# Performance work log

Hardware: AMD Instinct MI355X
Metric: run time of the kernel (lower is better)

## Reference

```python
import jax, jax.numpy as jnp
import numpy as np

R = 3                 # search_radius
S2 = (2 * R + 1) ** 2  # 49 correlation channels
VIS_PIXEL_SCALE = 0.1  # arcsec / pixel


def _interp_tokens(tokens, sh, sw, dh, dw):
    # tokens [B, N, D] on (sh, sw) grid -> (dh, dw) grid
    B, N, D = tokens.shape
    x = jnp.transpose(tokens, (0, 2, 1)).reshape(B, D, sh, sw)
    if (sh, sw) != (dh, dw):
        # torch F.interpolate bilinear align_corners=False == jax half-pixel bilinear
        x = jax.image.resize(x, (B, D, dh, dw), method='bilinear')
    return x  # [B, D, dh, dw]


def _l2norm(x, eps=1e-12):
    n = jnp.sqrt(jnp.sum(x * x, axis=1, keepdims=True))
    return x / jnp.maximum(n, eps)


def _corr_volume(q, ref):
    # q, ref: [B, D, H, W]; local cosine-similarity volume [B, S2, H, W]
    q = _l2norm(q)
    ref = _l2norm(ref)
    B, D, H, W = q.shape
    refp = jnp.pad(ref, ((0, 0), (0, 0), (R, R), (R, R)), mode='edge')  # replicate pad
    slices = [
        jnp.sum(q * jax.lax.dynamic_slice(refp, (0, 0, R + dy, R + dx), (B, D, H, W)), axis=1)
        for dy in range(-R, R + 1) for dx in range(-R, R + 1)
    ]
    return jnp.stack(slices, axis=1)


def _conv5(x, w, b):
    y = jax.lax.conv_general_dilated(x, w, (1, 1), 'SAME',
                                     dimension_numbers=('NCHW', 'OIHW', 'NCHW'))
    return y + b[None, :, None, None]


def _refine_net(x, w0, b0, w1, b1, w2, b2):
    h = jax.nn.gelu(_conv5(x, w0, b0), approximate=False)
    h = jax.nn.gelu(_conv5(h, w1, b1), approximate=False)
    return _conv5(h, w2, b2)


def setup_inputs() -> dict:
    key = jax.random.key(0)
    ks = jax.random.split(key, 8)
    B, D = 4, 256
    rubin_tokens = jax.random.normal(ks[0], (B, 64 * 64, D), dtype=jnp.float32)
    vis_tokens = jax.random.normal(ks[1], (B, 128 * 128, D), dtype=jnp.float32)
    in_ch = 2 + S2 + 1  # 52
    hid = 32
    def kaiming(k, shape):
        fan_in = shape[1] * shape[2] * shape[3]
        return jax.random.normal(k, shape, dtype=jnp.float32) / np.sqrt(fan_in)
    w0 = kaiming(ks[2], (hid, in_ch, 5, 5)); b0 = jnp.zeros((hid,), jnp.float32)
    w1 = kaiming(ks[3], (hid, hid, 5, 5));   b1 = jnp.zeros((hid,), jnp.float32)
    w2 = kaiming(ks[4], (2, hid, 5, 5));     b2 = jnp.zeros((2,), jnp.float32)
    log_temp = jnp.asarray(np.log(0.1), dtype=jnp.float32)
    return {
        'rubin_tokens': rubin_tokens, 'vis_tokens': vis_tokens,
        'w0': w0, 'b0': b0, 'w1': w1, 'b1': b1, 'w2': w2, 'b2': b2,
        'log_temp': log_temp,
        'rubin_h': 64, 'rubin_w': 64, 'vis_h': 128, 'vis_w': 128,
        'img_h': 2048, 'img_w': 2048,
    }


def reference(rubin_tokens, vis_tokens, w0, b0, w1, b1, w2, b2, log_temp,
              rubin_h, rubin_w, vis_h, vis_w, img_h, img_w):
    Hc, Wc = max(rubin_h, vis_h), max(rubin_w, vis_w)
    q = _interp_tokens(rubin_tokens, rubin_h, rubin_w, Hc, Wc)  # [B,D,Hc,Wc]
    k = _interp_tokens(vis_tokens, vis_h, vis_w, Hc, Wc)
    corr = _corr_volume(q, k)  # [B,S2,Hc,Wc]

    # soft-argmax over the (2R+1)^2 neighborhood
    coords = jnp.arange(-R, R + 1, dtype=corr.dtype)
    cy, cx = jnp.meshgrid(coords, coords, indexing='ij')
    cy = cy.reshape(1, S2, 1, 1)
    cx = cx.reshape(1, S2, 1, 1)
    temp = jnp.exp(log_temp)
    weights = jax.nn.softmax(corr / temp, axis=1)
    dy = jnp.sum(weights * cy, axis=1, keepdims=True)
    dx = jnp.sum(weights * cx, axis=1, keepdims=True)
    confidence = jnp.max(weights, axis=1, keepdims=True)
    raw_offsets = jnp.concatenate([dy, dx], axis=1)  # [B,2,Hc,Wc]

    x = jnp.concatenate([raw_offsets, corr, confidence], axis=1)  # [B,52,Hc,Wc]
    residual = _refine_net(x, w0, b0, w1, b1, w2, b2)
    refined = raw_offsets + residual

    sky_per_token_y = img_h * VIS_PIXEL_SCALE / Hc
    sky_per_token_x = img_w * VIS_PIXEL_SCALE / Wc
    dra = refined[:, 1:2] * sky_per_token_x
    ddec = refined[:, 0:1] * sky_per_token_y
    # [B,5,Hc,Wc]: dra, ddec, raw_dy, raw_dx, confidence
    return jnp.concatenate([dra, ddec, dy, dx, confidence], axis=1)
```

## Files before the change

kernel.cpp:

```cpp
#include <hip/hip_runtime.h>
#include <math.h>

#define Hh 128
#define Ww 128
#define Dd 256
#define Bb 4
#define HW (Hh*Ww)
#define NPIX (Bb*HW)
#define WP 132

typedef __attribute__((ext_vector_type(8))) short s16x8;
typedef __attribute__((ext_vector_type(4))) float f32x4;

__device__ __forceinline__ unsigned short f2bf(float f) {
    unsigned u = __float_as_uint(f);
    u += 0x7FFF + ((u >> 16) & 1);
    return (unsigned short)(u >> 16);
}

__device__ __forceinline__ float gelu_exact(float v) {
    return 0.5f * v * (1.0f + erff(v * 0.70710678118654752f));
}

__device__ __forceinline__ void ring_yx(int i, int& y, int& x) {
    if (i < 264) { y = i / 132; x = i - y * 132; }
    else if (i < 528) { int j = i - 264; int r = j / 132; y = 130 + r; x = j - r * 132; }
    else { int j = i - 528; y = 2 + (j >> 2); int m = j & 3; x = (m < 2) ? m : 128 + m; }
}

__global__ __launch_bounds__(256) void setup_norm(const float* __restrict__ w0,
                                                  const float* __restrict__ w1,
                                                  const float* __restrict__ w2,
                                                  unsigned short* __restrict__ wb0,
                                                  unsigned short* __restrict__ wb1,
                                                  unsigned short* __restrict__ wb2,
                                                  unsigned short* __restrict__ xbp,
                                                  unsigned short* __restrict__ h1p,
                                                  unsigned short* __restrict__ h2p,
                                                  const float* __restrict__ vis,
                                                  const float* __restrict__ rub,
                                                  unsigned short* __restrict__ kn,
                                                  unsigned short* __restrict__ qn) {
    __shared__ float stok[36 * 260];
    int tid = threadIdx.x;
    int blk = blockIdx.x;
    if (blk < 610) {
        int t = blk * 256 + tid;
        if (t < 66560) {
            uint4 z = (uint4){0, 0, 0, 0};
            if (t < 33280) {
                int img = t / 8320; int r = t - img * 8320; int px = r >> 3, g = r & 7;
                int y, x; ring_yx(px, y, x);
                *(uint4*)(xbp + ((size_t)(img * WP + y) * WP + x) * 64 + g * 8) = z;
            } else {
                int u = t - 33280;
                unsigned short* base = (u < 16640) ? h1p : h2p;
                int v = (u < 16640) ? u : u - 16640;
                int img = v / 4160; int r = v - img * 4160; int px = r >> 2, g = r & 3;
                int y, x; ring_yx(px, y, x);
                *(uint4*)(base + ((size_t)(img * WP + y) * WP + x) * 32 + g * 8) = z;
            }
            return;
        }
        int u = t - 66560;
        if (u < 51200) {
            int tap = u >> 11; int r = u & 2047; int n = r >> 6; int k = r & 63;
            wb0[u] = (k < 52) ? f2bf(w0[n * 1300 + k * 25 + tap]) : (unsigned short)0;
        } else if (u < 76800) {
            int v = u - 51200; int tap = v >> 10; int r = v & 1023; int n = r >> 5; int k = r & 31;
            wb1[v] = f2bf(w1[n * 800 + k * 25 + tap]);
        } else if (u < 89600) {
            int v = u - 76800; int tap = v >> 9; int r = v & 511; int n = r >> 5; int k = r & 31;
            wb2[v] = (n < 2) ? f2bf(w2[n * 800 + k * 25 + tap]) : (unsigned short)0;
        }
        return;
    }
    int nb = blk - 610;
    int g16 = tid >> 4, l = tid & 15;
    if (nb < 4096) {
        int pix = nb * 16 + g16;
        const float* base = vis + (size_t)pix * Dd + l * 4;
        float4 v[4];
#pragma unroll
        for (int i = 0; i < 4; i++) v[i] = *(const float4*)(base + i * 64);
        float ss = 0.f;
#pragma unroll
        for (int i = 0; i < 4; i++)
            ss += v[i].x * v[i].x + v[i].y * v[i].y + v[i].z * v[i].z + v[i].w * v[i].w;
#pragma unroll
        for (int o = 1; o <= 8; o <<= 1) ss += __shfl_xor(ss, o, 64);
        float inv = __builtin_amdgcn_rsqf(fmaxf(ss, 1e-24f));
        unsigned short* op = kn + (size_t)pix * Dd + l * 4;
#pragma unroll
        for (int i = 0; i < 4; i++) {
            ushort4 o4;
            o4.x = f2bf(v[i].x * inv); o4.y = f2bf(v[i].y * inv);
            o4.z = f2bf(v[i].z * inv); o4.w = f2bf(v[i].w * inv);
            *(ushort4*)(op + i * 64) = o4;
        }
    } else {
        int blk2 = nb - 4096;
        int b = blk2 >> 8;
        int rem = blk2 & 255;
        int ty = rem >> 4, tx = rem & 15;
        int oy0 = ty * 8, ox0 = tx * 8;
        int rb = ty * 4 - 1, cb = tx * 4 - 1;
#pragma unroll
        for (int i = 0; i < 9; i++) {
            int g = i * 256 + tid;
            int t = g >> 6, c = g & 63;
            int jy = t / 6, jx = t - jy * 6;
            int gy = min(max(rb + jy, 0), 63);
            int gx = min(max(cb + jx, 0), 63);
            *(float4*)&stok[t * 260 + c * 4] =
                *(const float4*)(rub + ((size_t)(b * 4096 + gy * 64 + gx)) * 256 + c * 4);
        }
        __syncthreads();
        for (int k = 0; k < 4; k++) {
            int pp = g16 * 4 + k;
            int r = pp >> 3, c2 = pp & 7;
            int yo = oy0 + r, xo = ox0 + c2;
            float sy = 0.5f * yo - 0.25f, sx = 0.5f * xo - 0.25f;
            float fyf = floorf(sy), fxf = floorf(sx);
            float fy = sy - fyf, fx = sx - fxf;
            int jy0 = (int)fyf - rb, jx0 = (int)fxf - cb;
            const float* t00 = &stok[(jy0 * 6 + jx0) * 260 + l * 4];
            const float* t01 = t00 + 260;
            const float* t10 = t00 + 6 * 260;
            const float* t11 = t10 + 260;
            float w00 = (1.f - fy) * (1.f - fx), w01 = (1.f - fy) * fx;
            float w10 = fy * (1.f - fx), w11 = fy * fx;
            float4 bv[4];
            float ss = 0.f;
#pragma unroll
            for (int i = 0; i < 4; i++) {
                float4 a = *(const float4*)(t00 + i * 64);
                float4 b1 = *(const float4*)(t01 + i * 64);
                float4 c = *(const float4*)(t10 + i * 64);
                float4 d = *(const float4*)(t11 + i * 64);
                float4 v;
                v.x = w00 * a.x + w01 * b1.x + w10 * c.x + w11 * d.x;
                v.y = w00 * a.y + w01 * b1.y + w10 * c.y + w11 * d.y;
                v.z = w00 * a.z + w01 * b1.z + w10 * c.z + w11 * d.z;
                v.w = w00 * a.w + w01 * b1.w + w10 * c.w + w11 * d.w;
                bv[i] = v;
                ss += v.x * v.x + v.y * v.y + v.z * v.z + v.w * v.w;
            }
#pragma unroll
            for (int o = 1; o <= 8; o <<= 1) ss += __shfl_xor(ss, o, 64);
            float inv = __builtin_amdgcn_rsqf(fmaxf(ss, 1e-24f));
            size_t pix = (size_t)(b << 14) + yo * 128 + xo;
            unsigned short* op = qn + pix * Dd + l * 4;
#pragma unroll
            for (int i = 0; i < 4; i++) {
                ushort4 o4;
                o4.x = f2bf(bv[i].x * inv); o4.y = f2bf(bv[i].y * inv);
                o4.z = f2bf(bv[i].z * inv); o4.w = f2bf(bv[i].w * inv);
                *(ushort4*)(op + i * 64) = o4;
            }
        }
    }
}

__global__ __launch_bounds__(512, 4) void corr_block(const unsigned short* __restrict__ qn,
                                                     const unsigned short* __restrict__ kn,
                                                     const float* __restrict__ log_temp,
                                                     unsigned short* __restrict__ xb,
                                                     float* __restrict__ out) {
    constexpr int ASMEM = 308 * 5 * 16;
    __shared__ char smem[ASMEM + 128 * 65 * 4];
    unsigned* sC = (unsigned*)(smem + ASMEM);
    int tid = threadIdx.x;
    int wid = tid >> 6, lane = tid & 63, l15 = lane & 15, quad = lane >> 4;
    int blk = blockIdx.x;
    int b = blk >> 7, rem = blk & 127;
    int y0 = (rem >> 3) << 3, x0 = (rem & 7) << 4;
    int y = y0 + wid;

#pragma unroll
    for (int i = 0; i < 3; i++) {
        int g = i * 512 + tid;
        int px = g / 12, ch = 52 + g - (g / 12) * 12;
        sC[px * 65 + ch] = 0u;
    }

    const unsigned short* src0; int dst0;
    const unsigned short* src1; int dst1;
    const unsigned short* src2; int dst2; bool hav2;
    {
        int g = tid;
        int px = g >> 2, sub = g & 3;
        int ry = px / 22, rx = px - ry * 22;
        int yy = min(max(y0 - 3 + ry, 0), 127);
        int xx = min(max(x0 - 3 + rx, 0), 127);
        src0 = kn + ((size_t)(b << 14) + yy * 128 + xx) * 256 + sub * 8;
        dst0 = (px * 5 + sub) * 16;
        g = 512 + tid;
        px = g >> 2; sub = g & 3;
        ry = px / 22; rx = px - ry * 22;
        yy = min(max(y0 - 3 + ry, 0), 127);
        xx = min(max(x0 - 3 + rx, 0), 127);
        src1 = kn + ((size_t)(b << 14) + yy * 128 + xx) * 256 + sub * 8;
        dst1 = (px * 5 + sub) * 16;
        g = 1024 + tid;
        hav2 = (g < 1232);
        int gc = hav2 ? g : 1231;
        px = gc >> 2; sub = gc & 3;
        ry = px / 22; rx = px - ry * 22;
        yy = min(max(y0 - 3 + ry, 0), 127);
        xx = min(max(x0 - 3 + rx, 0), 127);
        src2 = kn + ((size_t)(b << 14) + yy * 128 + xx) * 256 + sub * 8;
        dst2 = (px * 5 + sub) * 16;
    }
    int lpixoff[10];
#pragma unroll
    for (int f = 0; f < 10; f++) {
        int p = min(f * 16 + l15, 153);
        int pr = p / 22, pc = p - pr * 22;
        lpixoff[f] = (((wid + pr) * 22 + pc) * 5 + quad) * 16;
    }
    const unsigned short* aptr = qn + ((size_t)(b << 14) + y * 128 + x0 + l15) * 256 + quad * 8;

    f32x4 acc[10];
#pragma unroll
    for (int f = 0; f < 10; f++) acc[f] = (f32x4){0.f, 0.f, 0.f, 0.f};

    uint4 v0 = *(const uint4*)src0;
    uint4 v1 = *(const uint4*)src1;
    uint4 v2 = *(const uint4*)src2;
    s16x8 an = *(const s16x8*)aptr;
    for (int c = 0; c < 8; c++) {
        uint4 w0v = v0, w1v = v1, w2v = v2;
        s16x8 a = an;
        if (c < 7) {
            v0 = *(const uint4*)(src0 + (c + 1) * 32);
            v1 = *(const uint4*)(src1 + (c + 1) * 32);
            v2 = *(const uint4*)(src2 + (c + 1) * 32);
            an = *(const s16x8*)(aptr + (c + 1) * 32);
        }
        __syncthreads();
        *(uint4*)(smem + dst0) = w0v;
        *(uint4*)(smem + dst1) = w1v;
        if (hav2) *(uint4*)(smem + dst2) = w2v;
        __syncthreads();
#pragma unroll
        for (int f = 0; f < 10; f++) {
            s16x8 bf = *(const s16x8*)(smem + lpixoff[f]);
            acc[f] = __builtin_amdgcn_mfma_f32_16x16x32_bf16(a, bf, acc[f], 0, 0, 0);
        }
    }

    float inv_temp = expf(-log_temp[0]);
    float vmax[4] = {-1e30f, -1e30f, -1e30f, -1e30f};
#pragma unroll
    for (int f = 0; f < 10; f++) {
        int n = f * 16 + l15;
        if (n <= 153) {
            int dy = n / 22 - 3;
            int rx = n - (dy + 3) * 22;
#pragma unroll
            for (int i = 0; i < 4; i++) {
                int m = quad * 4 + i;
                int dx = rx - m - 3;
                if ((unsigned)(dx + 3) <= 6u) vmax[i] = fmaxf(vmax[i], acc[f][i]);
            }
        }
    }
#pragma unroll
    for (int o = 1; o <= 8; o <<= 1) {
#pragma unroll
        for (int i = 0; i < 4; i++) vmax[i] = fmaxf(vmax[i], __shfl_xor(vmax[i], o, 64));
    }
    float se[4] = {0, 0, 0, 0}, sey[4] = {0, 0, 0, 0}, sex[4] = {0, 0, 0, 0}, emax[4] = {0, 0, 0, 0};
#pragma unroll
    for (int f = 0; f < 10; f++) {
        int n = f * 16 + l15;
        if (n <= 153) {
            int dy = n / 22 - 3;
            int rx = n - (dy + 3) * 22;
#pragma unroll
            for (int i = 0; i < 4; i++) {
                int m = quad * 4 + i;
                int dx = rx - m - 3;
                if ((unsigned)(dx + 3) <= 6u) {
                    float v = acc[f][i];
                    float e = expf((v - vmax[i]) * inv_temp);
                    se[i] += e;
                    sey[i] += e * (float)dy;
                    sex[i] += e * (float)dx;
                    emax[i] = fmaxf(emax[i], e);
                    sC[(wid * 16 + m) * 65 + 2 + (dy + 3) * 7 + (dx + 3)] = (unsigned)f2bf(v);
                }
            }
        }
    }
#pragma unroll
    for (int o = 1; o <= 8; o <<= 1) {
#pragma unroll
        for (int i = 0; i < 4; i++) {
            se[i] += __shfl_xor(se[i], o, 64);
            sey[i] += __shfl_xor(sey[i], o, 64);
            sex[i] += __shfl_xor(sex[i], o, 64);
            emax[i] = fmaxf(emax[i], __shfl_xor(emax[i], o, 64));
        }
    }
    if (l15 == 0) {
#pragma unroll
        for (int i = 0; i < 4; i++) {
            int m = quad * 4 + i;
            float inv_se = 1.0f / se[i];
            float dyv = sey[i] * inv_se, dxv = sex[i] * inv_se, conf = emax[i] * inv_se;
            int px = wid * 16 + m;
            sC[px * 65 + 0] = (unsigned)f2bf(dyv);
            sC[px * 65 + 1] = (unsigned)f2bf(dxv);
            sC[px * 65 + 51] = (unsigned)f2bf(conf);
            float* op = out + (size_t)b * 5 * HW + y * 128 + x0 + m;
            op[2 * HW] = dyv; op[3 * HW] = dxv; op[4 * HW] = conf;
        }
    }
    __syncthreads();
#pragma unroll
    for (int i = 0; i < 2; i++) {
        int t2 = i * 512 + tid;
        int px = t2 >> 3, seg = t2 & 7;
        const unsigned* sp = sC + px * 65 + seg * 8;
        uint4 o;
        o.x = sp[0] | (sp[1] << 16);
        o.y = sp[2] | (sp[3] << 16);
        o.z = sp[4] | (sp[5] << 16);
        o.w = sp[6] | (sp[7] << 16);
        unsigned short* dst = xb + ((size_t)(b * WP + y0 + (px >> 4) + 2) * WP + x0 + (px & 15) + 2) * 64 + seg * 8;
        *(uint4*)dst = o;
    }
}

template <int KS, int OC, bool GELU>
__global__ __launch_bounds__(512, 4) void conv_tile(const unsigned short* __restrict__ in,
                                                    const unsigned short* __restrict__ wb,
                                                    const float* __restrict__ bias,
                                                    unsigned short* __restrict__ outp) {
    constexpr int ICP = KS * 32;
    constexpr int NF = OC / 16;
    constexpr int ABYTES = 240 * 64;
    constexpr int WROWS = 25 * OC;
    constexpr int WGRAN = WROWS * 4;
    __shared__ char smem[ABYTES + WROWS * 64];
    int tid = threadIdx.x;
    int wv = tid >> 6, lane = tid & 63, l15 = lane & 15, quad = lane >> 4;
    int blk = blockIdx.x;
    int b = blk >> 7, rem = blk & 127;
    int ty = rem >> 3, tx = rem & 7;
    int y0 = ty * 8, x0 = tx * 16;

    f32x4 acc[NF];
#pragma unroll
    for (int g = 0; g < NF; g++) acc[g] = (f32x4){0.f, 0.f, 0.f, 0.f};

    for (int ks = 0; ks < KS; ks++) {
        __syncthreads();
#pragma unroll
        for (int i = 0; i < 2; i++) {
            int g = i * 512 + tid;
            if (g < 960) {
                int px = g >> 2, sub = g & 3;
                int r = px / 20, c = px - r * 20;
                *(uint4*)(smem + px * 64 + (((sub ^ (px >> 1)) & 3) << 4)) =
                    *(const uint4*)(in + ((size_t)(b * WP + y0 + r) * WP + x0 + c) * ICP + ks * 32 + sub * 8);
            }
        }
#pragma unroll
        for (int i = 0; i < (WGRAN + 511) / 512; i++) {
            int g = i * 512 + tid;
            if (g < WGRAN) {
                int nl = g >> 2, sub = g & 3;
                *(uint4*)(smem + ABYTES + nl * 64 + (((sub ^ (nl >> 1)) & 3) << 4)) =
                    *(const uint4*)(wb + (size_t)nl * ICP + ks * 32 + sub * 8);
            }
        }
        __syncthreads();
#pragma unroll
        for (int ky = 0; ky < 5; ky++) {
#pragma unroll
            for (int kx = 0; kx < 5; kx++) {
                int px = (wv + ky) * 20 + l15 + kx;
                s16x8 a = *(const s16x8*)(smem + px * 64 + (((quad ^ (px >> 1)) & 3) << 4));
#pragma unroll
                for (int g = 0; g < NF; g++) {
                    int row = (ky * 5 + kx) * OC + g * 16 + l15;
                    s16x8 bf = *(const s16x8*)(smem + ABYTES + row * 64 + (((quad ^ (row >> 1)) & 3) << 4));
                    acc[g] = __builtin_amdgcn_mfma_f32_16x16x32_bf16(a, bf, acc[g], 0, 0, 0);
                }
            }
        }
    }
    size_t orow = ((size_t)(b * WP + y0 + wv + 2) * WP + x0 + 2) * OC;
#pragma unroll
    for (int g = 0; g < NF; g++) {
        float bv = bias[g * 16 + l15];
#pragma unroll
        for (int r = 0; r < 4; r++) {
            int m = quad * 4 + r;
            float v = acc[g][r] + bv;
            if (GELU) v = gelu_exact(v);
            outp[orow + (size_t)m * OC + g * 16 + l15] = f2bf(v);
        }
    }
}

__global__ __launch_bounds__(512, 4) void conv_final_tile(const unsigned short* __restrict__ in,
                                                          const unsigned short* __restrict__ wb,
                                                          const float* __restrict__ bias,
                                                          float* __restrict__ out) {
    constexpr int ICP = 32, OC = 16;
    constexpr int ABYTES = 240 * 64;
    constexpr int WROWS = 25 * OC;
    constexpr int WGRAN = WROWS * 4;
    __shared__ char smem[ABYTES + WROWS * 64];
    int tid = threadIdx.x;
    int wv = tid >> 6, lane = tid & 63, l15 = lane & 15, quad = lane >> 4;
    int blk = blockIdx.x;
    int b = blk >> 7, rem = blk & 127;
    int ty = rem >> 3, tx = rem & 7;
    int y0 = ty * 8, x0 = tx * 16;

#pragma unroll
    for (int i = 0; i < 2; i++) {
        int g = i * 512 + tid;
        if (g < 960) {
            int px = g >> 2, sub = g & 3;
            int r = px / 20, c = px - r * 20;
            *(uint4*)(smem + px * 64 + (((sub ^ (px >> 1)) & 3) << 4)) =
                *(const uint4*)(in + ((size_t)(b * WP + y0 + r) * WP + x0 + c) * ICP + sub * 8);
        }
    }
#pragma unroll
    for (int i = 0; i < 4; i++) {
        int g = i * 512 + tid;
        if (g < WGRAN) {
            int nl = g >> 2, sub = g & 3;
            *(uint4*)(smem + ABYTES + nl * 64 + (((sub ^ (nl >> 1)) & 3) << 4)) =
                *(const uint4*)(wb + (size_t)nl * ICP + sub * 8);
        }
    }
    __syncthreads();
    f32x4 acc = (f32x4){0.f, 0.f, 0.f, 0.f};
#pragma unroll
    for (int ky = 0; ky < 5; ky++) {
#pragma unroll
        for (int kx = 0; kx < 5; kx++) {
            int px = (wv + ky) * 20 + l15 + kx;
            s16x8 a = *(const s16x8*)(smem + px * 64 + (((quad ^ (px >> 1)) & 3) << 4));
            int row = (ky * 5 + kx) * OC + l15;
            s16x8 bf = *(const s16x8*)(smem + ABYTES + row * 64 + (((quad ^ (row >> 1)) & 3) << 4));
            acc = __builtin_amdgcn_mfma_f32_16x16x32_bf16(a, bf, acc, 0, 0, 0);
        }
    }
    if (l15 < 2) {
        float bv = bias[l15];
#pragma unroll
        for (int r = 0; r < 4; r++) {
            int m = quad * 4 + r;
            size_t p5 = (size_t)b * 5 * HW + (y0 + wv) * Ww + x0 + m;
            float a = acc[r] + bv;
            if (l15 == 0) {
                float dyv = out[p5 + 2 * HW];
                out[p5 + HW] = (dyv + a) * 1.6f;
            } else {
                float dxv = out[p5 + 3 * HW];
                out[p5] = (dxv + a) * 1.6f;
            }
        }
    }
}

extern "C" void kernel_launch(void* const* d_in, const int* in_sizes, int n_in,
                              void* d_out, int out_size, void* d_ws, size_t ws_size,
                              hipStream_t stream) {
    const float* rub = (const float*)d_in[0];
    const float* vis = (const float*)d_in[1];
    const float* w0 = (const float*)d_in[2];
    const float* b0 = (const float*)d_in[3];
    const float* w1 = (const float*)d_in[4];
    const float* b1 = (const float*)d_in[5];
    const float* w2 = (const float*)d_in[6];
    const float* b2 = (const float*)d_in[7];
    const float* log_temp = (const float*)d_in[8];
    float* out = (float*)d_out;

    char* ws = (char*)d_ws;
    size_t off = 0;
    const size_t PADPIX = (size_t)Bb * WP * WP;
    unsigned short* kn = (unsigned short*)(ws + off); off += (size_t)NPIX * Dd * 2;
    unsigned short* qn = (unsigned short*)(ws + off); off += (size_t)NPIX * Dd * 2;
    unsigned short* xbp = (unsigned short*)(ws + off); off += PADPIX * 64 * 2;
    unsigned short* h1p = (unsigned short*)(ws + off); off += PADPIX * 32 * 2;
    unsigned short* h2p = (unsigned short*)(ws + off); off += PADPIX * 32 * 2;
    unsigned short* wb0 = (unsigned short*)(ws + off); off += 51200 * 2;
    unsigned short* wb1 = (unsigned short*)(ws + off); off += 25600 * 2;
    unsigned short* wb2 = (unsigned short*)(ws + off); off += 12800 * 2;

    setup_norm<<<5730, 256, 0, stream>>>(w0, w1, w2, wb0, wb1, wb2,
                                         xbp, h1p, h2p, vis, rub, kn, qn);
    corr_block<<<512, 512, 0, stream>>>(qn, kn, log_temp, xbp, out);
    conv_tile<2, 32, true><<<512, 512, 0, stream>>>(xbp, wb0, b0, h1p);
    conv_tile<1, 32, true><<<512, 512, 0, stream>>>(h1p, wb1, b1, h2p);
    conv_final_tile<<<512, 512, 0, stream>>>(h2p, wb2, b2, out);
}
```

Baseline: 192.0 us.

## Widen correlation K-chunks to 64 and vectorize bf16 normalization stores

The correlation kernel now stages 64 channels of the reference window per step instead of 32, so it makes 4 trips with barriers instead of 8, and issues two MFMAs per fragment per trip. The shared buffer is reused for the sC scratch after an extra barrier, so LDS use drops. The normalization kernels now give each pixel 32 lanes and write packed 16-byte bf16 stores instead of 8-byte ones. The trade-off is more live prefetch registers in the correlation loop and a larger per-step staging footprint.

```diff
diff --git a/kernel.cpp b/kernel.cpp
--- a/kernel.cpp
+++ b/kernel.cpp
@@ -76,28 +76,36 @@
         return;
     }
     int nb = blk - 610;
-    int g16 = tid >> 4, l = tid & 15;
+    int g32 = tid >> 5, l = tid & 31;
     if (nb < 4096) {
-        int pix = nb * 16 + g16;
-        const float* base = vis + (size_t)pix * Dd + l * 4;
-        float4 v[4];
-#pragma unroll
-        for (int i = 0; i < 4; i++) v[i] = *(const float4*)(base + i * 64);
-        float ss = 0.f;
-#pragma unroll
-        for (int i = 0; i < 4; i++)
-            ss += v[i].x * v[i].x + v[i].y * v[i].y + v[i].z * v[i].z + v[i].w * v[i].w;
-#pragma unroll
-        for (int o = 1; o <= 8; o <<= 1) ss += __shfl_xor(ss, o, 64);
-        float inv = __builtin_amdgcn_rsqf(fmaxf(ss, 1e-24f));
-        unsigned short* op = kn + (size_t)pix * Dd + l * 4;
-#pragma unroll
-        for (int i = 0; i < 4; i++) {
-            ushort4 o4;
-            o4.x = f2bf(v[i].x * inv); o4.y = f2bf(v[i].y * inv);
-            o4.z = f2bf(v[i].z * inv); o4.w = f2bf(v[i].w * inv);
-            *(ushort4*)(op + i * 64) = o4;
-        }
+        int pix0 = nb * 16 + g32 * 2;
+        const float* base0 = vis + (size_t)pix0 * Dd + l * 4;
+        float4 a0 = *(const float4*)(base0);
+        float4 b0 = *(const float4*)(base0 + 128);
+        float4 a1 = *(const float4*)(base0 + 256);
+        float4 b1 = *(const float4*)(base0 + 384);
+        float ss0 = a0.x * a0.x + a0.y * a0.y + a0.z * a0.z + a0.w * a0.w +
+                    b0.x * b0.x + b0.y * b0.y + b0.z * b0.z + b0.w * b0.w;
+        float ss1 = a1.x * a1.x + a1.y * a1.y + a1.z * a1.z + a1.w * a1.w +
+                    b1.x * b1.x + b1.y * b1.y + b1.z * b1.z + b1.w * b1.w;
+#pragma unroll
+        for (int o = 1; o <= 16; o <<= 1) {
+            ss0 += __shfl_xor(ss0, o, 64);
+            ss1 += __shfl_xor(ss1, o, 64);
+        }
+        float inv0 = __builtin_amdgcn_rsqf(fmaxf(ss0, 1e-24f));
+        float inv1 = __builtin_amdgcn_rsqf(fmaxf(ss1, 1e-24f));
+        uint4 o0, o1;
+        o0.x = f2bf(a0.x * inv0) | ((unsigned)f2bf(a0.y * inv0) << 16);
+        o0.y = f2bf(a0.z * inv0) | ((unsigned)f2bf(a0.w * inv0) << 16);
+        o0.z = f2bf(b0.x * inv0) | ((unsigned)f2bf(b0.y * inv0) << 16);
+        o0.w = f2bf(b0.z * inv0) | ((unsigned)f2bf(b0.w * inv0) << 16);
+        o1.x = f2bf(a1.x * inv1) | ((unsigned)f2bf(a1.y * inv1) << 16);
+        o1.y = f2bf(a1.z * inv1) | ((unsigned)f2bf(a1.w * inv1) << 16);
+        o1.z = f2bf(b1.x * inv1) | ((unsigned)f2bf(b1.y * inv1) << 16);
+        o1.w = f2bf(b1.z * inv1) | ((unsigned)f2bf(b1.w * inv1) << 16);
+        *(uint4*)(kn + (size_t)pix0 * Dd + l * 8) = o0;
+        *(uint4*)(kn + (size_t)(pix0 + 1) * Dd + l * 8) = o1;
     } else {
         int blk2 = nb - 4096;
         int b = blk2 >> 8;
@@ -116,48 +124,51 @@
                 *(const float4*)(rub + ((size_t)(b * 4096 + gy * 64 + gx)) * 256 + c * 4);
         }
         __syncthreads();
-        for (int k = 0; k < 4; k++) {
-            int pp = g16 * 4 + k;
+        for (int k = 0; k < 8; k++) {
+            int pp = g32 * 8 + k;
             int r = pp >> 3, c2 = pp & 7;
             int yo = oy0 + r, xo = ox0 + c2;
             float sy = 0.5f * yo - 0.25f, sx = 0.5f * xo - 0.25f;
             float fyf = floorf(sy), fxf = floorf(sx);
             float fy = sy - fyf, fx = sx - fxf;
             int jy0 = (int)fyf - rb, jx0 = (int)fxf - cb;
-            const float* t00 = &stok[(jy0 * 6 + jx0) * 260 + l * 4];
+            const float* t00 = &stok[(jy0 * 6 + jx0) * 260];
             const float* t01 = t00 + 260;
             const float* t10 = t00 + 6 * 260;
             const float* t11 = t10 + 260;
             float w00 = (1.f - fy) * (1.f - fx), w01 = (1.f - fy) * fx;
             float w10 = fy * (1.f - fx), w11 = fy * fx;
-            float4 bv[4];
-            float ss = 0.f;
-#pragma unroll
-            for (int i = 0; i < 4; i++) {
-                float4 a = *(const float4*)(t00 + i * 64);
-                float4 b1 = *(const float4*)(t01 + i * 64);
-                float4 c = *(const float4*)(t10 + i * 64);
-                float4 d = *(const float4*)(t11 + i * 64);
-                float4 v;
-                v.x = w00 * a.x + w01 * b1.x + w10 * c.x + w11 * d.x;
-                v.y = w00 * a.y + w01 * b1.y + w10 * c.y + w11 * d.y;
-                v.z = w00 * a.z + w01 * b1.z + w10 * c.z + w11 * d.z;
-                v.w = w00 * a.w + w01 * b1.w + w10 * c.w + w11 * d.w;
-                bv[i] = v;
-                ss += v.x * v.x + v.y * v.y + v.z * v.z + v.w * v.w;
-            }
-#pragma unroll
-            for (int o = 1; o <= 8; o <<= 1) ss += __shfl_xor(ss, o, 64);
+            float4 av, bv;
+            {
+                float4 A0 = *(const float4*)(t00 + l * 4);
+                float4 B0 = *(const float4*)(t01 + l * 4);
+                float4 C0 = *(const float4*)(t10 + l * 4);
+                float4 D0 = *(const float4*)(t11 + l * 4);
+                av.x = w00 * A0.x + w01 * B0.x + w10 * C0.x + w11 * D0.x;
+                av.y = w00 * A0.y + w01 * B0.y + w10 * C0.y + w11 * D0.y;
+                av.z = w00 * A0.z + w01 * B0.z + w10 * C0.z + w11 * D0.z;
+                av.w = w00 * A0.w + w01 * B0.w + w10 * C0.w + w11 * D0.w;
+                float4 A1 = *(const float4*)(t00 + 128 + l * 4);
+                float4 B1 = *(const float4*)(t01 + 128 + l * 4);
+                float4 C1 = *(const float4*)(t10 + 128 + l * 4);
+                float4 D1 = *(const float4*)(t11 + 128 + l * 4);
+                bv.x = w00 * A1.x + w01 * B1.x + w10 * C1.x + w11 * D1.x;
+                bv.y = w00 * A1.y + w01 * B1.y + w10 * C1.y + w11 * D1.y;
+                bv.z = w00 * A1.z + w01 * B1.z + w10 * C1.z + w11 * D1.z;
+                bv.w = w00 * A1.w + w01 * B1.w + w10 * C1.w + w11 * D1.w;
+            }
+            float ss = av.x * av.x + av.y * av.y + av.z * av.z + av.w * av.w +
+                       bv.x * bv.x + bv.y * bv.y + bv.z * bv.z + bv.w * bv.w;
+#pragma unroll
+            for (int o = 1; o <= 16; o <<= 1) ss += __shfl_xor(ss, o, 64);
             float inv = __builtin_amdgcn_rsqf(fmaxf(ss, 1e-24f));
             size_t pix = (size_t)(b << 14) + yo * 128 + xo;
-            unsigned short* op = qn + pix * Dd + l * 4;
-#pragma unroll
-            for (int i = 0; i < 4; i++) {
-                ushort4 o4;
-                o4.x = f2bf(bv[i].x * inv); o4.y = f2bf(bv[i].y * inv);
-                o4.z = f2bf(bv[i].z * inv); o4.w = f2bf(bv[i].w * inv);
-                *(ushort4*)(op + i * 64) = o4;
-            }
+            uint4 o4;
+            o4.x = f2bf(av.x * inv) | ((unsigned)f2bf(av.y * inv) << 16);
+            o4.y = f2bf(av.z * inv) | ((unsigned)f2bf(av.w * inv) << 16);
+            o4.z = f2bf(bv.x * inv) | ((unsigned)f2bf(bv.y * inv) << 16);
+            o4.w = f2bf(bv.z * inv) | ((unsigned)f2bf(bv.w * inv) << 16);
+            *(uint4*)(qn + pix * Dd + l * 8) = o4;
         }
     }
 }
@@ -167,9 +178,8 @@
                                                      const float* __restrict__ log_temp,
                                                      unsigned short* __restrict__ xb,
                                                      float* __restrict__ out) {
-    constexpr int ASMEM = 308 * 5 * 16;
-    __shared__ char smem[ASMEM + 128 * 65 * 4];
-    unsigned* sC = (unsigned*)(smem + ASMEM);
+    __shared__ __align__(16) char smem[320 * 144];
+    unsigned* sC = (unsigned*)smem;
     int tid = threadIdx.x;
     int wid = tid >> 6, lane = tid & 63, l15 = lane & 15, quad = lane >> 4;
     int blk = blockIdx.x;
@@ -177,77 +187,76 @@
     int y0 = (rem >> 3) << 3, x0 = (rem & 7) << 4;
     int y = y0 + wid;
 
+    int soff[5], dstf[5];
+#pragma unroll
+    for (int i = 0; i < 5; i++) {
+        int g = i * 512 + tid;
+        int px = g >> 3, sub = g & 7;
+        int pxc = min(px, 307);
+        int ry = pxc / 22, rx = pxc - ry * 22;
+        int yy = min(max(y0 - 3 + ry, 0), 127);
+        int xx = min(max(x0 - 3 + rx, 0), 127);
+        soff[i] = ((b << 14) + yy * 128 + xx) * 256 + sub * 8;
+        dstf[i] = px * 144 + sub * 16;
+    }
+    int lpixoff[10];
+#pragma unroll
+    for (int f = 0; f < 10; f++) {
+        int p = min(f * 16 + l15, 153);
+        int pr = p / 22, pc = p - pr * 22;
+        lpixoff[f] = ((wid + pr) * 22 + pc) * 144 + quad * 16;
+    }
+    int aoff = ((b << 14) + y * 128 + x0 + l15) * 256 + quad * 8;
+
+    f32x4 acc[10];
+#pragma unroll
+    for (int f = 0; f < 10; f++) acc[f] = (f32x4){0.f, 0.f, 0.f, 0.f};
+
+    uint4 st0 = *(const uint4*)(kn + soff[0]);
+    uint4 st1 = *(const uint4*)(kn + soff[1]);
+    uint4 st2 = *(const uint4*)(kn + soff[2]);
+    uint4 st3 = *(const uint4*)(kn + soff[3]);
+    uint4 st4 = *(const uint4*)(kn + soff[4]);
+    s16x8 a0 = *(const s16x8*)(qn + aoff);
+    s16x8 a1 = *(const s16x8*)(qn + aoff + 32);
+    for (int c4 = 0; c4 < 4; c4++) {
+        uint4 w0 = st0, w1 = st1, w2 = st2, w3 = st3, w4 = st4;
+        s16x8 wa0 = a0, wa1 = a1;
+        if (c4 < 3) {
+            int co = (c4 + 1) * 64;
+            st0 = *(const uint4*)(kn + soff[0] + co);
+            st1 = *(const uint4*)(kn + soff[1] + co);
+            st2 = *(const uint4*)(kn + soff[2] + co);
+            st3 = *(const uint4*)(kn + soff[3] + co);
+            st4 = *(const uint4*)(kn + soff[4] + co);
+            a0 = *(const s16x8*)(qn + aoff + co);
+            a1 = *(const s16x8*)(qn + aoff + co + 32);
+        }
+        __syncthreads();
+        *(uint4*)(smem + dstf[0]) = w0;
+        *(uint4*)(smem + dstf[1]) = w1;
+        *(uint4*)(smem + dstf[2]) = w2;
+        *(uint4*)(smem + dstf[3]) = w3;
+        *(uint4*)(smem + dstf[4]) = w4;
+        __syncthreads();
+#pragma unroll
+        for (int f = 0; f < 10; f++) {
+            s16x8 bf = *(const s16x8*)(smem + lpixoff[f]);
+            acc[f] = __builtin_amdgcn_mfma_f32_16x16x32_bf16(wa0, bf, acc[f], 0, 0, 0);
+        }
+#pragma unroll
+        for (int f = 0; f < 10; f++) {
+            s16x8 bf = *(const s16x8*)(smem + lpixoff[f] + 64);
+            acc[f] = __builtin_amdgcn_mfma_f32_16x16x32_bf16(wa1, bf, acc[f], 0, 0, 0);
+        }
+    }
+    __syncthreads();
+
 #pragma unroll
     for (int i = 0; i < 3; i++) {
         int g = i * 512 + tid;
         int px = g / 12, ch = 52 + g - (g / 12) * 12;
         sC[px * 65 + ch] = 0u;
-    }
-
-    const unsigned short* src0; int dst0;
-    const unsigned short* src1; int dst1;
-    const unsigned short* src2; int dst2; bool hav2;
-    {
-        int g = tid;
-        int px = g >> 2, sub = g & 3;
-        int ry = px / 22, rx = px - ry * 22;
-        int yy = min(max(y0 - 3 + ry, 0), 127);
-        int xx = min(max(x0 - 3 + rx, 0), 127);
-        src0 = kn + ((size_t)(b << 14) + yy * 128 + xx) * 256 + sub * 8;
-        dst0 = (px * 5 + sub) * 16;
-        g = 512 + tid;
-        px = g >> 2; sub = g & 3;
-        ry = px / 22; rx = px - ry * 22;
-        yy = min(max(y0 - 3 + ry, 0), 127);
-        xx = min(max(x0 - 3 + rx, 0), 127);
-        src1 = kn + ((size_t)(b << 14) + yy * 128 + xx) * 256 + sub * 8;
-        dst1 = (px * 5 + sub) * 16;
-        g = 1024 + tid;
-        hav2 = (g < 1232);
-        int gc = hav2 ? g : 1231;
-        px = gc >> 2; sub = gc & 3;
-        ry = px / 22; rx = px - ry * 22;
-        yy = min(max(y0 - 3 + ry, 0), 127);
-        xx = min(max(x0 - 3 + rx, 0), 127);
-        src2 = kn + ((size_t)(b << 14) + yy * 128 + xx) * 256 + sub * 8;
-        dst2 = (px * 5 + sub) * 16;
-    }
-    int lpixoff[10];
-#pragma unroll
-    for (int f = 0; f < 10; f++) {
-        int p = min(f * 16 + l15, 153);
-        int pr = p / 22, pc = p - pr * 22;
-        lpixoff[f] = (((wid + pr) * 22 + pc) * 5 + quad) * 16;
-    }
-    const unsigned short* aptr = qn + ((size_t)(b << 14) + y * 128 + x0 + l15) * 256 + quad * 8;
-
-    f32x4 acc[10];
-#pragma unroll
-    for (int f = 0; f < 10; f++) acc[f] = (f32x4){0.f, 0.f, 0.f, 0.f};
-
-    uint4 v0 = *(const uint4*)src0;
-    uint4 v1 = *(const uint4*)src1;
-    uint4 v2 = *(const uint4*)src2;
-    s16x8 an = *(const s16x8*)aptr;
-    for (int c = 0; c < 8; c++) {
-        uint4 w0v = v0, w1v = v1, w2v = v2;
-        s16x8 a = an;
-        if (c < 7) {
-            v0 = *(const uint4*)(src0 + (c + 1) * 32);
-            v1 = *(const uint4*)(src1 + (c + 1) * 32);
-            v2 = *(const uint4*)(src2 + (c + 1) * 32);
-            an = *(const s16x8*)(aptr + (c + 1) * 32);
-        }
-        __syncthreads();
-        *(uint4*)(smem + dst0) = w0v;
-        *(uint4*)(smem + dst1) = w1v;
-        if (hav2) *(uint4*)(smem + dst2) = w2v;
-        __syncthreads();
-#pragma unroll
-        for (int f = 0; f < 10; f++) {
-            s16x8 bf = *(const s16x8*)(smem + lpixoff[f]);
-            acc[f] = __builtin_amdgcn_mfma_f32_16x16x32_bf16(a, bf, acc[f], 0, 0, 0);
-        }
     }
 
     float inv_temp = expf(-log_temp[0]);
```

New measurement: 195.0 us. No clear change (+1.6%).

## Fuse second conv and final conv into one kernel with halo recompute

Applied to the files above, without the earlier changes.

Merges the second 5x5 conv (GELU) and the final 5x5 conv into a single kernel. Each tile loads a wider halo of h1 (padding 4 instead of 2), computes h2 for a 12x20 region into shared memory, masks out-of-image positions to zero, then runs the final conv directly from LDS. This removes the h2 global round trip and one launch. The cost is redundant halo computation, extra LDS use (66KB) and staged weight reloads, which may reduce occupancy.

```diff
diff --git a/kernel.cpp b/kernel.cpp
--- a/kernel.cpp
+++ b/kernel.cpp
@@ -8,6 +8,7 @@
 #define HW (Hh*Ww)
 #define NPIX (Bb*HW)
 #define WP 132
+#define WP1 136
 
 typedef __attribute__((ext_vector_type(8))) short s16x8;
 typedef __attribute__((ext_vector_type(4))) float f32x4;
@@ -26,6 +27,12 @@
     if (i < 264) { y = i / 132; x = i - y * 132; }
     else if (i < 528) { int j = i - 264; int r = j / 132; y = 130 + r; x = j - r * 132; }
     else { int j = i - 528; y = 2 + (j >> 2); int m = j & 3; x = (m < 2) ? m : 128 + m; }
+}
+
+__device__ __forceinline__ void ring4_yx(int i, int& y, int& x) {
+    if (i < 544) { y = i / 136; x = i - y * 136; }
+    else if (i < 1088) { int j = i - 544; int r = j / 136; y = 132 + r; x = j - r * 136; }
+    else { int j = i - 1088; y = 4 + (j >> 3); int m = j & 7; x = (m < 4) ? m : 128 + m; }
 }
 
 __global__ __launch_bounds__(256) void setup_norm(const float* __restrict__ w0,
@@ -36,7 +43,6 @@
                                                   unsigned short* __restrict__ wb2,
                                                   unsigned short* __restrict__ xbp,
                                                   unsigned short* __restrict__ h1p,
-                                                  unsigned short* __restrict__ h2p,
                                                   const float* __restrict__ vis,
                                                   const float* __restrict__ rub,
                                                   unsigned short* __restrict__ kn,
@@ -44,25 +50,23 @@
     __shared__ float stok[36 * 260];
     int tid = threadIdx.x;
     int blk = blockIdx.x;
-    if (blk < 610) {
+    if (blk < 612) {
         int t = blk * 256 + tid;
-        if (t < 66560) {
-            uint4 z = (uint4){0, 0, 0, 0};
-            if (t < 33280) {
-                int img = t / 8320; int r = t - img * 8320; int px = r >> 3, g = r & 7;
-                int y, x; ring_yx(px, y, x);
-                *(uint4*)(xbp + ((size_t)(img * WP + y) * WP + x) * 64 + g * 8) = z;
-            } else {
-                int u = t - 33280;
-                unsigned short* base = (u < 16640) ? h1p : h2p;
-                int v = (u < 16640) ? u : u - 16640;
-                int img = v / 4160; int r = v - img * 4160; int px = r >> 2, g = r & 3;
-                int y, x; ring_yx(px, y, x);
-                *(uint4*)(base + ((size_t)(img * WP + y) * WP + x) * 32 + g * 8) = z;
-            }
+        uint4 z = (uint4){0, 0, 0, 0};
+        if (t < 33280) {
+            int img = t / 8320; int r = t - img * 8320; int px = r >> 3, g = r & 7;
+            int y, x; ring_yx(px, y, x);
+            *(uint4*)(xbp + ((size_t)(img * WP + y) * WP + x) * 64 + g * 8) = z;
             return;
         }
-        int u = t - 66560;
+        if (t < 67072) {
+            int u2 = t - 33280;
+            int img = u2 / 8448; int r = u2 - img * 8448; int px = r >> 2, g = r & 3;
+            int y, x; ring4_yx(px, y, x);
+            *(uint4*)(h1p + ((size_t)(img * WP1 + y) * WP1 + x) * 32 + g * 8) = z;
+            return;
+        }
+        int u = t - 67072;
         if (u < 51200) {
             int tap = u >> 11; int r = u & 2047; int n = r >> 6; int k = r & 63;
             wb0[u] = (k < 52) ? f2bf(w0[n * 1300 + k * 25 + tap]) : (unsigned short)0;
@@ -75,7 +79,7 @@
         }
         return;
     }
-    int nb = blk - 610;
+    int nb = blk - 612;
     int g16 = tid >> 4, l = tid & 15;
     if (nb < 4096) {
         int pix = nb * 16 + g16;
@@ -334,12 +338,11 @@
     }
 }
 
-template <int KS, int OC, bool GELU>
-__global__ __launch_bounds__(512, 4) void conv_tile(const unsigned short* __restrict__ in,
-                                                    const unsigned short* __restrict__ wb,
-                                                    const float* __restrict__ bias,
-                                                    unsigned short* __restrict__ outp) {
-    constexpr int ICP = KS * 32;
+__global__ __launch_bounds__(512, 4) void conv1_tile(const unsigned short* __restrict__ in,
+                                                     const unsigned short* __restrict__ wb,
+                                                     const float* __restrict__ bias,
+                                                     unsigned short* __restrict__ outp) {
+    constexpr int KS = 2, OC = 32, ICP = 64;
     constexpr int NF = OC / 16;
     constexpr int ABYTES = 240 * 64;
     constexpr int WROWS = 25 * OC;
@@ -393,29 +396,29 @@
             }
         }
     }
-    size_t orow = ((size_t)(b * WP + y0 + wv + 2) * WP + x0 + 2) * OC;
+    size_t orow = ((size_t)(b * WP1 + y0 + wv + 4) * WP1 + x0 + 4) * OC;
 #pragma unroll
     for (int g = 0; g < NF; g++) {
         float bv = bias[g * 16 + l15];
 #pragma unroll
         for (int r = 0; r < 4; r++) {
             int m = quad * 4 + r;
-            float v = acc[g][r] + bv;
-            if (GELU) v = gelu_exact(v);
+            float v = gelu_exact(acc[g][r] + bv);
             outp[orow + (size_t)m * OC + g * 16 + l15] = f2bf(v);
         }
     }
 }
 
-__global__ __launch_bounds__(512, 4) void conv_final_tile(const unsigned short* __restrict__ in,
-                                                          const unsigned short* __restrict__ wb,
-                                                          const float* __restrict__ bias,
-                                                          float* __restrict__ out) {
-    constexpr int ICP = 32, OC = 16;
-    constexpr int ABYTES = 240 * 64;
-    constexpr int WROWS = 25 * OC;
-    constexpr int WGRAN = WROWS * 4;
-    __shared__ char smem[ABYTES + WROWS * 64];
+__global__ __launch_bounds__(512, 4) void conv2_final(const unsigned short* __restrict__ h1,
+                                                      const unsigned short* __restrict__ wb1,
+                                                      const float* __restrict__ b1,
+                                                      const unsigned short* __restrict__ wb2,
+                                                      const float* __restrict__ b2,
+                                                      float* __restrict__ out) {
+    constexpr int H1B = 384 * 64;
+    constexpr int WOFF = H1B;
+    constexpr int H2OFF = H1B + 26624;
+    __shared__ __align__(16) char smem[66560];
     int tid = threadIdx.x;
     int wv = tid >> 6, lane = tid & 63, l15 = lane & 15, quad = lane >> 4;
     int blk = blockIdx.x;
@@ -423,45 +426,129 @@
     int ty = rem >> 3, tx = rem & 7;
     int y0 = ty * 8, x0 = tx * 16;
 
-#pragma unroll
-    for (int i = 0; i < 2; i++) {
+    int p0u = wv * 16 + l15;
+    int p1u = (8 + wv) * 16 + l15;
+    int r0 = p0u / 20, c0 = p0u - r0 * 20;
+    int r1 = p1u / 20, c1 = p1u - r1 * 20;
+    bool has1 = ((8 + wv) < 15);
+
+#pragma unroll
+    for (int i = 0; i < 3; i++) {
         int g = i * 512 + tid;
-        if (g < 960) {
-            int px = g >> 2, sub = g & 3;
-            int r = px / 20, c = px - r * 20;
-            *(uint4*)(smem + px * 64 + (((sub ^ (px >> 1)) & 3) << 4)) =
-                *(const uint4*)(in + ((size_t)(b * WP + y0 + r) * WP + x0 + c) * ICP + sub * 8);
-        }
+        int px = g >> 2, sub = g & 3;
+        int r = px / 24, c = px - r * 24;
+        *(uint4*)(smem + px * 64 + (((sub ^ (px >> 1)) & 3) << 4)) =
+            *(const uint4*)(h1 + ((size_t)(b * WP1 + y0 + r) * WP1 + x0 + c) * 32 + sub * 8);
     }
 #pragma unroll
     for (int i = 0; i < 4; i++) {
         int g = i * 512 + tid;
-        if (g < WGRAN) {
+        if (g < 1664) {
             int nl = g >> 2, sub = g & 3;
-            *(uint4*)(smem + ABYTES + nl * 64 + (((sub ^ (nl >> 1)) & 3) << 4)) =
-                *(const uint4*)(wb + (size_t)nl * ICP + sub * 8);
+            *(uint4*)(smem + WOFF + nl * 64 + (((sub ^ (nl >> 1)) & 3) << 4)) =
+                *(const uint4*)(wb1 + (size_t)nl * 32 + sub * 8);
         }
     }
     __syncthreads();
-    f32x4 acc = (f32x4){0.f, 0.f, 0.f, 0.f};
-#pragma unroll
-    for (int ky = 0; ky < 5; ky++) {
-#pragma unroll
-        for (int kx = 0; kx < 5; kx++) {
-            int px = (wv + ky) * 20 + l15 + kx;
+
+    f32x4 acc2[2][2];
+#pragma unroll
+    for (int s = 0; s < 2; s++) { acc2[s][0] = (f32x4){0,0,0,0}; acc2[s][1] = (f32x4){0,0,0,0}; }
+
+    for (int t = 0; t < 13; t++) {
+        int tap = t, ky = tap / 5, kx = tap - ky * 5;
+        int lr0 = t * 32 + l15, lr1 = t * 32 + 16 + l15;
+        s16x8 wf0 = *(const s16x8*)(smem + WOFF + lr0 * 64 + (((quad ^ (lr0 >> 1)) & 3) << 4));
+        s16x8 wf1 = *(const s16x8*)(smem + WOFF + lr1 * 64 + (((quad ^ (lr1 >> 1)) & 3) << 4));
+        {
+            int px = (r0 + ky) * 24 + c0 + kx;
             s16x8 a = *(const s16x8*)(smem + px * 64 + (((quad ^ (px >> 1)) & 3) << 4));
-            int row = (ky * 5 + kx) * OC + l15;
-            s16x8 bf = *(const s16x8*)(smem + ABYTES + row * 64 + (((quad ^ (row >> 1)) & 3) << 4));
-            acc = __builtin_amdgcn_mfma_f32_16x16x32_bf16(a, bf, acc, 0, 0, 0);
-        }
+            acc2[0][0] = __builtin_amdgcn_mfma_f32_16x16x32_bf16(a, wf0, acc2[0][0], 0, 0, 0);
+            acc2[0][1] = __builtin_amdgcn_mfma_f32_16x16x32_bf16(a, wf1, acc2[0][1], 0, 0, 0);
+        }
+        if (has1) {
+            int px = (r1 + ky) * 24 + c1 + kx;
+            s16x8 a = *(const s16x8*)(smem + px * 64 + (((quad ^ (px >> 1)) & 3) << 4));
+            acc2[1][0] = __builtin_amdgcn_mfma_f32_16x16x32_bf16(a, wf0, acc2[1][0], 0, 0, 0);
+            acc2[1][1] = __builtin_amdgcn_mfma_f32_16x16x32_bf16(a, wf1, acc2[1][1], 0, 0, 0);
+        }
+    }
+    __syncthreads();
+#pragma unroll
+    for (int i = 0; i < 3; i++) {
+        int g = i * 512 + tid;
+        int nl = g >> 2, sub = g & 3;
+        *(uint4*)(smem + WOFF + nl * 64 + (((sub ^ (nl >> 1)) & 3) << 4)) =
+            *(const uint4*)(wb1 + (size_t)(416 + nl) * 32 + sub * 8);
+    }
+    __syncthreads();
+    for (int t = 0; t < 12; t++) {
+        int tap = 13 + t, ky = tap / 5, kx = tap - ky * 5;
+        int lr0 = t * 32 + l15, lr1 = t * 32 + 16 + l15;
+        s16x8 wf0 = *(const s16x8*)(smem + WOFF + lr0 * 64 + (((quad ^ (lr0 >> 1)) & 3) << 4));
+        s16x8 wf1 = *(const s16x8*)(smem + WOFF + lr1 * 64 + (((quad ^ (lr1 >> 1)) & 3) << 4));
+        {
+            int px = (r0 + ky) * 24 + c0 + kx;
+            s16x8 a = *(const s16x8*)(smem + px * 64 + (((quad ^ (px >> 1)) & 3) << 4));
+            acc2[0][0] = __builtin_amdgcn_mfma_f32_16x16x32_bf16(a, wf0, acc2[0][0], 0, 0, 0);
+            acc2[0][1] = __builtin_amdgcn_mfma_f32_16x16x32_bf16(a, wf1, acc2[0][1], 0, 0, 0);
+        }
+        if (has1) {
+            int px = (r1 + ky) * 24 + c1 + kx;
+            s16x8 a = *(const s16x8*)(smem + px * 64 + (((quad ^ (px >> 1)) & 3) << 4));
+            acc2[1][0] = __builtin_amdgcn_mfma_f32_16x16x32_bf16(a, wf0, acc2[1][0], 0, 0, 0);
+            acc2[1][1] = __builtin_amdgcn_mfma_f32_16x16x32_bf16(a, wf1, acc2[1][1], 0, 0, 0);
+        }
+    }
+#pragma unroll
+    for (int s = 0; s < 2; s++) {
+        int u = s * 8 + wv;
+        if (u < 15) {
+#pragma unroll
+            for (int g2 = 0; g2 < 2; g2++) {
+                float bvv = b1[g2 * 16 + l15];
+                int n = g2 * 16 + l15, gran = n >> 3;
+#pragma unroll
+                for (int rr = 0; rr < 4; rr++) {
+                    int p = u * 16 + quad * 4 + rr;
+                    int r2 = p / 20, c2 = p - r2 * 20;
+                    int gy = y0 - 2 + r2, gx = x0 - 2 + c2;
+                    float v = gelu_exact(acc2[s][g2][rr] + bvv);
+                    unsigned short o = ((unsigned)gy < 128u && (unsigned)gx < 128u)
+                                           ? f2bf(v) : (unsigned short)0;
+                    *(unsigned short*)(smem + H2OFF + p * 64 +
+                                       (((gran ^ (p >> 1)) & 3) << 4) + (n & 7) * 2) = o;
+                }
+            }
+        }
+    }
+    __syncthreads();
+#pragma unroll
+    for (int i = 0; i < 4; i++) {
+        int g = i * 512 + tid;
+        if (g < 1600) {
+            int nl = g >> 2, sub = g & 3;
+            *(uint4*)(smem + WOFF + nl * 64 + (((sub ^ (nl >> 1)) & 3) << 4)) =
+                *(const uint4*)(wb2 + (size_t)nl * 32 + sub * 8);
+        }
+    }
+    __syncthreads();
+    f32x4 acc3 = (f32x4){0.f, 0.f, 0.f, 0.f};
+    for (int t = 0; t < 25; t++) {
+        int ky = t / 5, kx = t - ky * 5;
+        int p3 = (wv + ky) * 20 + l15 + kx;
+        s16x8 a = *(const s16x8*)(smem + H2OFF + p3 * 64 + (((quad ^ (p3 >> 1)) & 3) << 4));
+        int lr = t * 16 + l15;
+        s16x8 bf = *(const s16x8*)(smem + WOFF + lr * 64 + (((quad ^ (lr >> 1)) & 3) << 4));
+        acc3 = __builtin_amdgcn_mfma_f32_16x16x32_bf16(a, bf, acc3, 0, 0, 0);
     }
     if (l15 < 2) {
-        float bv = bias[l15];
-#pragma unroll
-        for (int r = 0; r < 4; r++) {
-            int m = quad * 4 + r;
+        float bv = b2[l15];
+#pragma unroll
+        for (int rr = 0; rr < 4; rr++) {
+            int m = quad * 4 + rr;
             size_t p5 = (size_t)b * 5 * HW + (y0 + wv) * Ww + x0 + m;
-            float a = acc[r] + bv;
+            float a = acc3[rr] + bv;
             if (l15 == 0) {
                 float dyv = out[p5 + 2 * HW];
                 out[p5 + HW] = (dyv + a) * 1.6f;
@@ -490,19 +577,18 @@
     char* ws = (char*)d_ws;
     size_t off = 0;
     const size_t PADPIX = (size_t)Bb * WP * WP;
+    const size_t PADPIX1 = (size_t)Bb * WP1 * WP1;
     unsigned short* kn = (unsigned short*)(ws + off); off += (size_t)NPIX * Dd * 2;
     unsigned short* qn = (unsigned short*)(ws + off); off += (size_t)NPIX * Dd * 2;
     unsigned short* xbp = (unsigned short*)(ws + off); off += PADPIX * 64 * 2;
-    unsigned short* h1p = (unsigned short*)(ws + off); off += PADPIX * 32 * 2;
-    unsigned short* h2p = (unsigned short*)(ws + off); off += PADPIX * 32 * 2;
+    unsigned short* h1p = (unsigned short*)(ws + off); off += PADPIX1 * 32 * 2;
     unsigned short* wb0 = (unsigned short*)(ws + off); off += 51200 * 2;
     unsigned short* wb1 = (unsigned short*)(ws + off); off += 25600 * 2;
     unsigned short* wb2 = (unsigned short*)(ws + off); off += 12800 * 2;
 
-    setup_norm<<<5730, 256, 0, stream>>>(w0, w1, w2, wb0, wb1, wb2,
-                                         xbp, h1p, h2p, vis, rub, kn, qn);
+    setup_norm<<<5732, 256, 0, stream>>>(w0, w1, w2, wb0, wb1, wb2,
+                                         xbp, h1p, vis, rub, kn, qn);
     corr_block<<<512, 512, 0, stream>>>(qn, kn, log_temp, xbp, out);
-    conv_tile<2, 32, true><<<512, 512, 0, stream>>>(xbp, wb0, b0, h1p);
-    conv_tile<1, 32, true><<<512, 512, 0, stream>>>(h1p, wb1, b1, h2p);
-    conv_final_tile<<<512, 512, 0, stream>>>(h2p, wb2, b2, out);
-}
+    conv1_tile<<<512, 512, 0, stream>>>(xbp, wb0, b0, h1p);
+    conv2_final<<<512, 512, 0, stream>>>(h1p, wb1, b1, wb2, b2, out);
+}
```

Result: no change. 194.5 us (+1.3%).
